# Performance work log

Measured on AMD Instinct MI355X. Metric: run time of the kernel, lower is better.

Reference implementation:

```python
import jax, jax.numpy as jnp
import numpy as np

B, Q, C = 128, 192, 512   # batch, num_queries (= num_targets per sample), num_classes
COST_CLASS = 1.0
BIG = jnp.float32(1e30)


def _lsap_col4row(cost):
    """Exact linear sum assignment (Jonker-Volgenant shortest augmenting path,
    same algorithm as scipy.optimize.linear_sum_assignment).
    cost: [n, n] float32. Returns col4row[i] = column assigned to row i (int32)."""
    n = cost.shape[0]

    def solve_row(cur_row, state):
        u, v, row4col, col4row = state

        # Dijkstra-like search for the shortest augmenting path from cur_row.
        def dj_cond(s):
            return s[6] < 0  # sink not found yet

        def dj_body(s):
            i, minVal, SR, SC, spc, path, sink = s
            SR = SR.at[i].set(True)
            r = minVal + cost[i] - u[i] - v          # reduced path costs, [n]
            upd = (~SC) & (r < spc)
            path = jnp.where(upd, i, path)
            spc = jnp.where(upd, r, spc)
            masked = jnp.where(SC, BIG, spc)
            j = jnp.argmin(masked).astype(jnp.int32)
            minVal = masked[j]
            SC = SC.at[j].set(True)
            unassigned = row4col[j] < 0
            sink = jnp.where(unassigned, j, jnp.int32(-1))
            i = jnp.where(unassigned, i, row4col[j])
            return i, minVal, SR, SC, spc, path, sink

        init = (jnp.asarray(cur_row, jnp.int32), jnp.float32(0.0),
                jnp.zeros(n, bool), jnp.zeros(n, bool),
                jnp.full(n, BIG, jnp.float32), jnp.zeros(n, jnp.int32),
                jnp.int32(-1))
        _, minVal, SR, SC, spc, path, sink = jax.lax.while_loop(dj_cond, dj_body, init)

        # Dual variable updates.
        u = u.at[cur_row].add(minVal)
        others = SR & (jnp.arange(n) != cur_row)   # assigned rows visited in the search
        u = u + jnp.where(others, minVal - spc[col4row], 0.0)
        v = v - jnp.where(SC, minVal - spc, 0.0)

        # Augment along the stored path from sink back to cur_row.
        def aug_cond(s):
            return ~s[3]

        def aug_body(s):
            j, r4c, c4r, _ = s
            i = path[j]
            r4c = r4c.at[j].set(i)
            nj = c4r[i]
            c4r = c4r.at[i].set(j)
            return nj, r4c, c4r, i == cur_row

        _, row4col, col4row, _ = jax.lax.while_loop(
            aug_cond, aug_body, (sink, row4col, col4row, jnp.bool_(False)))
        return u, v, row4col, col4row

    state = (jnp.zeros(n, jnp.float32), jnp.zeros(n, jnp.float32),
             jnp.full(n, -1, jnp.int32), jnp.full(n, -1, jnp.int32))
    _, _, _, col4row = jax.lax.fori_loop(0, n, solve_row, state)
    return col4row


def _match(predictions, targets):
    """BipartiteMatching: cost[b,q,j] = -softmax(pred)[b,q,targets[b,j]];
    per-sample Hungarian. Returns col4row: [B, Q] (row q matched to target col)."""
    prob = jax.nn.softmax(predictions, axis=-1)            # [B,Q,C]
    tgt = targets.astype(jnp.int32)
    cost = -jax.vmap(lambda p, t: p[:, t])(prob, tgt)      # [B,Q,Q]
    return jax.vmap(_lsap_col4row)(COST_CLASS * cost)      # [B,Q]


def setup_inputs() -> dict:
    key = jax.random.key(0)
    k1, k2 = jax.random.split(key)
    predictions = jax.random.normal(k1, (B, Q, C), dtype=jnp.float32)
    targets = jax.random.randint(k2, (B, Q), 0, C).astype(jnp.int64)
    return {"predictions": predictions, "targets": targets}


def reference(predictions, targets):
    # Matching is done under no_grad in the original module.
    col4row = _match(jax.lax.stop_gradient(predictions), targets)          # [B,Q]
    # Since matching is square, every query is matched; the num_classes fill
    # in the original is always fully overwritten.
    target_classes = jnp.take_along_axis(targets, col4row.astype(targets.dtype), axis=1)
    logp = jax.nn.log_softmax(predictions, axis=-1)                        # [B,Q,C]
    nll = -jnp.take_along_axis(logp, target_classes[..., None].astype(jnp.int32), axis=-1)
    return jnp.mean(nll)  # F.cross_entropy with default mean reduction over B*Q
```

## Files before the change

### kernel.cpp

```cpp
#include <hip/hip_runtime.h>
#include <math.h>


#define BB 128
#define QQ 192
#define CC 512
#define NBIG 1e30f

template<int CTRL>
__device__ __forceinline__ int dpp_mov(int x) {
    return __builtin_amdgcn_update_dpp(x, x, CTRL, 0xf, 0xf, false);
}

__device__ __forceinline__ int readlane_i(int v, int l) {
    return __builtin_amdgcn_readlane(v, l);
}
__device__ __forceinline__ float readlane_f(float v, int l) {
    return __int_as_float(__builtin_amdgcn_readlane(__float_as_int(v), l));
}
__device__ __forceinline__ unsigned umin_(unsigned a, unsigned b) { return a < b ? a : b; }

__device__ __forceinline__ float wave_max64(float x) {
    x = fmaxf(x, __int_as_float(dpp_mov<0x111>(__float_as_int(x))));
    x = fmaxf(x, __int_as_float(dpp_mov<0x112>(__float_as_int(x))));
    x = fmaxf(x, __int_as_float(dpp_mov<0x114>(__float_as_int(x))));
    x = fmaxf(x, __int_as_float(dpp_mov<0x118>(__float_as_int(x))));
    x = fmaxf(x, __int_as_float(dpp_mov<0x142>(__float_as_int(x))));
    x = fmaxf(x, __int_as_float(dpp_mov<0x143>(__float_as_int(x))));
    return __int_as_float(__builtin_amdgcn_readlane(__float_as_int(x), 63));
}
__device__ __forceinline__ float wave_sum64(float x) {
    x += __int_as_float(dpp_mov<0x111>(__float_as_int(x)));
    x += __int_as_float(dpp_mov<0x112>(__float_as_int(x)));
    x += __int_as_float(dpp_mov<0x114>(__float_as_int(x)));
    x += __int_as_float(dpp_mov<0x118>(__float_as_int(x)));
    x += __int_as_float(dpp_mov<0x142>(__float_as_int(x)));
    x += __int_as_float(dpp_mov<0x143>(__float_as_int(x)));
    return __int_as_float(__builtin_amdgcn_readlane(__float_as_int(x), 63));
}

__device__ __forceinline__ unsigned wave_min_pk(unsigned x) {
    x = umin_(x, (unsigned)dpp_mov<0x111>((int)x));
    x = umin_(x, (unsigned)dpp_mov<0x112>((int)x));
    x = umin_(x, (unsigned)dpp_mov<0x114>((int)x));
    x = umin_(x, (unsigned)dpp_mov<0x118>((int)x));
    unsigned a = (unsigned)readlane_i((int)x, 15);
    unsigned b = (unsigned)readlane_i((int)x, 31);
    unsigned c = (unsigned)readlane_i((int)x, 47);
    unsigned d = (unsigned)readlane_i((int)x, 63);
    return umin_(umin_(a, b), umin_(c, d));
}

__device__ __forceinline__ unsigned fkey(float f) {
    unsigned b = __float_as_uint(f);
    return b ^ (((unsigned)((int)b >> 31)) | 0x80000000u);
}

#define GET_I3(a, idx) readlane_i((((idx)>>6)==0) ? a##0 : ((((idx)>>6)==1) ? a##1 : a##2), (idx)&63)
#define GET_F3(a, idx) readlane_f((((idx)>>6)==0) ? a##0 : ((((idx)>>6)==1) ? a##1 : a##2), (idx)&63)
#define SET_I3(a, idx, val) do { const int _s=(idx)>>6, _l=(idx)&63; \
    if (_s==0) { if (lane==_l) a##0=(val); } \
    else if (_s==1) { if (lane==_l) a##1=(val); } \
    else { if (lane==_l) a##2=(val); } } while(0)

__launch_bounds__(256)
__global__ void hungarian_kernel(const float* __restrict__ pred,
                                 const int* __restrict__ targets,
                                 float* __restrict__ ws_part) {
    const int b = blockIdx.x;
    const int lane = threadIdx.x & 63;
    const int wv = threadIdx.x >> 6;

    extern __shared__ float smem[];
    float* cost    = smem;
    float* spc_lds = cost + QQ * QQ;
    float* lse_lds = spc_lds + QQ;
    int*   tgt_lds = (int*)(lse_lds + QQ);

    const int t0 = targets[b * QQ + lane];
    const int t1 = targets[b * QQ + lane + 64];
    const int t2 = targets[b * QQ + lane + 128];
    if (wv == 0) { tgt_lds[lane] = t0; tgt_lds[lane + 64] = t1; tgt_lds[lane + 128] = t2; }

    const float* predb = pred + (size_t)b * QQ * CC;
    {
        const int q0 = wv * 48, q1 = q0 + 48;
        float x[8];
        #pragma unroll
        for (int k = 0; k < 8; k++) x[k] = predb[(size_t)q0 * CC + lane + 64 * k];
        for (int q = q0; q < q1; q++) {
            const float* row = predb + (size_t)q * CC;
            float g0 = row[t0], g1 = row[t1], g2 = row[t2];
            float xn[8];
            if (q + 1 < q1) {
                const float* nrow = row + CC;
                #pragma unroll
                for (int k = 0; k < 8; k++) xn[k] = nrow[lane + 64 * k];
            }
            float mx = x[0];
            #pragma unroll
            for (int k = 1; k < 8; k++) mx = fmaxf(mx, x[k]);
            mx = wave_max64(mx);
            float s = 0.f;
            #pragma unroll
            for (int k = 0; k < 8; k++) s += expf(x[k] - mx);
            s = wave_sum64(s);
            float lse = mx + logf(s);
            if (lane == 0) lse_lds[q] = lse;
            cost[q * QQ + lane]       = -expf(g0 - lse);
            cost[q * QQ + lane + 64]  = -expf(g1 - lse);
            cost[q * QQ + lane + 128] = -expf(g2 - lse);
            #pragma unroll
            for (int k = 0; k < 8; k++) x[k] = xn[k];
        }
    }
    __syncthreads();
    if (wv != 0) return;

    float u0 = 0.f, u1 = 0.f, u2 = 0.f;
    float v0 = 0.f, v1 = 0.f, v2 = 0.f;
    int   c0 = -1, c1 = -1, c2 = -1;
    int   r0 = -1, r1 = -1, r2 = -1;

    for (int cur = 0; cur < QQ; cur++) {
        float spc0 = NBIG, spc1 = NBIG, spc2 = NBIG;
        int   p0 = 0, p1 = 0, p2 = 0;
        int   sc0 = 0, sc1 = 0, sc2 = 0;
        unsigned long long SRm0 = 0, SRm1 = 0, SRm2 = 0;
        int   i = cur;
        float minVal = 0.f;
        int   sink;

        while (true) {
            {
                const int is = i >> 6, il = i & 63;
                if (is == 0)      SRm0 |= 1ull << il;
                else if (is == 1) SRm1 |= 1ull << il;
                else              SRm2 |= 1ull << il;
            }
            const float* crow = cost + i * QQ;
            const float cA = crow[lane];
            const float cB = crow[lane + 64];
            const float cD = crow[lane + 128];
            const float ui = GET_F3(u, i);

            float rA = ((minVal + cA) - ui) - v0;  rA = sc0 ? NBIG : rA;
            if (rA < spc0) { spc0 = rA; p0 = i; }
            float rB = ((minVal + cB) - ui) - v1;  rB = sc1 ? NBIG : rB;
            if (rB < spc1) { spc1 = rB; p1 = i; }
            float rD = ((minVal + cD) - ui) - v2;  rD = sc2 ? NBIG : rD;
            if (rD < spc2) { spc2 = rD; p2 = i; }

            unsigned pkA = sc0 ? 0xFFFFFFFFu : ((fkey(spc0) & 0xFFFFFF00u) | (unsigned)lane);
            unsigned pkB = sc1 ? 0xFFFFFFFFu : ((fkey(spc1) & 0xFFFFFF00u) | (unsigned)(lane + 64));
            unsigned pkD = sc2 ? 0xFFFFFFFFu : ((fkey(spc2) & 0xFFFFFF00u) | (unsigned)(lane + 128));
            const unsigned pk = wave_min_pk(umin_(umin_(pkA, pkB), pkD));
            const int jstar = (int)(pk & 255u);
            const int os = jstar >> 6, ol = jstar & 63;

            minVal = readlane_f(os == 0 ? spc0 : (os == 1 ? spc1 : spc2), ol);
            sc0 |= (jstar == lane);
            sc1 |= (jstar == lane + 64);
            sc2 |= (jstar == lane + 128);
            const int rj = readlane_i(os == 0 ? r0 : (os == 1 ? r1 : r2), ol);
            if (rj < 0) { sink = jstar; break; }
            i = rj;
        }

        u0 += (cur == lane) ? minVal : 0.f;
        u1 += (cur == lane + 64) ? minVal : 0.f;
        u2 += (cur == lane + 128) ? minVal : 0.f;
        spc_lds[lane] = spc0; spc_lds[lane + 64] = spc1; spc_lds[lane + 128] = spc2;
        const int f0 = (int)((SRm0 >> lane) & 1ull);
        const int f1 = (int)((SRm1 >> lane) & 1ull);
        const int f2 = (int)((SRm2 >> lane) & 1ull);
        if (f0 && lane != cur)         u0 += minVal - spc_lds[c0];
        if (f1 && (lane + 64) != cur)  u1 += minVal - spc_lds[c1];
        if (f2 && (lane + 128) != cur) u2 += minVal - spc_lds[c2];
        if (sc0) v0 -= (minVal - spc0);
        if (sc1) v1 -= (minVal - spc1);
        if (sc2) v2 -= (minVal - spc2);

        int j = sink;
        while (true) {
            const int pj = GET_I3(p, j);
            SET_I3(r, j, pj);
            const int nj = GET_I3(c, pj);
            SET_I3(c, pj, j);
            if (pj == cur) break;
            j = nj;
        }
    }

    float part = 0.f;
    {
        const int tc0 = tgt_lds[c0], tc1 = tgt_lds[c1], tc2 = tgt_lds[c2];
        part += lse_lds[lane]       - predb[(size_t)lane * CC + tc0];
        part += lse_lds[lane + 64]  - predb[(size_t)(lane + 64) * CC + tc1];
        part += lse_lds[lane + 128] - predb[(size_t)(lane + 128) * CC + tc2];
    }
    part = wave_sum64(part);
    if (lane == 0) ws_part[b] = part;
}

__launch_bounds__(64)
__global__ void reduce_kernel(const float* __restrict__ ws_part,
                              float* __restrict__ out) {
    int lane = threadIdx.x;
    float s = ws_part[lane] + ws_part[lane + 64];
    s = wave_sum64(s);
    if (lane == 0) out[0] = s / (float)(BB * QQ);
}

extern "C" void kernel_launch(void* const* d_in, const int* in_sizes, int n_in,
                              void* d_out, int out_size, void* d_ws, size_t ws_size,
                              hipStream_t stream) {
    const float* pred = (const float*)d_in[0];
    const int* targets = (const int*)d_in[1];
    float* out = (float*)d_out;
    float* ws = (float*)d_ws;

    const int lds_bytes = (QQ * QQ + 3 * QQ) * (int)sizeof(float);

    hipLaunchKernelGGL(hungarian_kernel, dim3(BB), dim3(256), lds_bytes, stream,
                       pred, targets, ws);
    hipLaunchKernelGGL(reduce_kernel, dim3(1), dim3(64), 0, stream, ws, out);
}
```

Baseline: 837.1 us.

## Pack assigned-row index into argmin key to remove readlanes on critical path

The Dijkstra inner loop now keeps a per-column packed key that carries the column's assigned row plus one in its low byte. A single wave min-reduction therefore yields the next row directly, without dependent readlanes of the row4col registers. The minVal readlane and the SC marking are deferred into the next iteration using ballots on matching keys. The reduced-cost arithmetic is also refactored to hoist the shared minVal-ui term. This shortens the serial dependency chain per step, at the cost of extra ballots and changed tie-breaking (the low bits now hold row ids instead of column ids), which could alter the assignment when keys tie.

```diff
diff --git a/kernel.cpp b/kernel.cpp
--- a/kernel.cpp
+++ b/kernel.cpp
@@ -119,17 +119,22 @@
 
     float u0 = 0.f, u1 = 0.f, u2 = 0.f;
     float v0 = 0.f, v1 = 0.f, v2 = 0.f;
-    int   c0 = -1, c1 = -1, c2 = -1;
-    int   r0 = -1, r1 = -1, r2 = -1;
+    int   xx0 = -1, xx1 = -1, xx2 = -1;
+    int   yy0 = -1, yy1 = -1, yy2 = -1;
 
     for (int cur = 0; cur < QQ; cur++) {
         float spc0 = NBIG, spc1 = NBIG, spc2 = NBIG;
         int   p0 = 0, p1 = 0, p2 = 0;
         int   sc0 = 0, sc1 = 0, sc2 = 0;
+        unsigned k0 = 0xFFFFFFFFu, k1 = 0xFFFFFFFFu, k2 = 0xFFFFFFFFu;
         unsigned long long SRm0 = 0, SRm1 = 0, SRm2 = 0;
+        const unsigned yf0 = (unsigned)(yy0 + 1);
+        const unsigned yf1 = (unsigned)(yy1 + 1);
+        const unsigned yf2 = (unsigned)(yy2 + 1);
         int   i = cur;
         float minVal = 0.f;
         int   sink;
+        unsigned mn = 0xFFFFFFFFu;
 
         while (true) {
             {
@@ -142,29 +147,49 @@
             const float cA = crow[lane];
             const float cB = crow[lane + 64];
             const float cD = crow[lane + 128];
+
+            if (mn != 0xFFFFFFFFu) {
+                const int m0 = (k0 == mn), m1 = (k1 == mn), m2 = (k2 == mn);
+                const unsigned long long b0 = __ballot(m0);
+                const unsigned long long b1 = __ballot(m1);
+                const unsigned long long b2 = __ballot(m2);
+                if (b0)      minVal = readlane_f(spc0, __ffsll(b0) - 1);
+                else if (b1) minVal = readlane_f(spc1, __ffsll(b1) - 1);
+                else         minVal = readlane_f(spc2, __ffsll(b2) - 1);
+                sc0 |= m0; sc1 |= m1; sc2 |= m2;
+                k0 = m0 ? 0xFFFFFFFFu : k0;
+                k1 = m1 ? 0xFFFFFFFFu : k1;
+                k2 = m2 ? 0xFFFFFFFFu : k2;
+            }
             const float ui = GET_F3(u, i);
-
-            float rA = ((minVal + cA) - ui) - v0;  rA = sc0 ? NBIG : rA;
+            const float fs = minVal - ui;
+            const float sv0 = sc0 ? NBIG : fs - v0;
+            const float sv1 = sc1 ? NBIG : fs - v1;
+            const float sv2 = sc2 ? NBIG : fs - v2;
+
+            const float rA = cA + sv0;
+            const float rB = cB + sv1;
+            const float rD = cD + sv2;
             if (rA < spc0) { spc0 = rA; p0 = i; }
-            float rB = ((minVal + cB) - ui) - v1;  rB = sc1 ? NBIG : rB;
             if (rB < spc1) { spc1 = rB; p1 = i; }
-            float rD = ((minVal + cD) - ui) - v2;  rD = sc2 ? NBIG : rD;
             if (rD < spc2) { spc2 = rD; p2 = i; }
-
-            unsigned pkA = sc0 ? 0xFFFFFFFFu : ((fkey(spc0) & 0xFFFFFF00u) | (unsigned)lane);
-            unsigned pkB = sc1 ? 0xFFFFFFFFu : ((fkey(spc1) & 0xFFFFFF00u) | (unsigned)(lane + 64));
-            unsigned pkD = sc2 ? 0xFFFFFFFFu : ((fkey(spc2) & 0xFFFFFF00u) | (unsigned)(lane + 128));
-            const unsigned pk = wave_min_pk(umin_(umin_(pkA, pkB), pkD));
-            const int jstar = (int)(pk & 255u);
-            const int os = jstar >> 6, ol = jstar & 63;
-
-            minVal = readlane_f(os == 0 ? spc0 : (os == 1 ? spc1 : spc2), ol);
-            sc0 |= (jstar == lane);
-            sc1 |= (jstar == lane + 64);
-            sc2 |= (jstar == lane + 128);
-            const int rj = readlane_i(os == 0 ? r0 : (os == 1 ? r1 : r2), ol);
-            if (rj < 0) { sink = jstar; break; }
-            i = rj;
+            k0 = umin_(k0, (fkey(rA) & 0xFFFFFF00u) | yf0);
+            k1 = umin_(k1, (fkey(rB) & 0xFFFFFF00u) | yf1);
+            k2 = umin_(k2, (fkey(rD) & 0xFFFFFF00u) | yf2);
+
+            mn = wave_min_pk(umin_(umin_(k0, k1), k2));
+            const int rjf = (int)(mn & 255u);
+            if (rjf == 0) {
+                const unsigned long long b0 = __ballot(k0 == mn);
+                const unsigned long long b1 = __ballot(k1 == mn);
+                const unsigned long long b2 = __ballot(k2 == mn);
+                int ol;
+                if (b0)      { ol = __ffsll(b0) - 1; sink = ol;       minVal = readlane_f(spc0, ol); }
+                else if (b1) { ol = __ffsll(b1) - 1; sink = ol + 64;  minVal = readlane_f(spc1, ol); }
+                else         { ol = __ffsll(b2) - 1; sink = ol + 128; minVal = readlane_f(spc2, ol); }
+                break;
+            }
+            i = rjf - 1;
         }
 
         u0 += (cur == lane) ? minVal : 0.f;
@@ -174,9 +199,9 @@
         const int f0 = (int)((SRm0 >> lane) & 1ull);
         const int f1 = (int)((SRm1 >> lane) & 1ull);
         const int f2 = (int)((SRm2 >> lane) & 1ull);
-        if (f0 && lane != cur)         u0 += minVal - spc_lds[c0];
-        if (f1 && (lane + 64) != cur)  u1 += minVal - spc_lds[c1];
-        if (f2 && (lane + 128) != cur) u2 += minVal - spc_lds[c2];
+        if (f0 && lane != cur)         u0 += minVal - spc_lds[xx0];
+        if (f1 && (lane + 64) != cur)  u1 += minVal - spc_lds[xx1];
+        if (f2 && (lane + 128) != cur) u2 += minVal - spc_lds[xx2];
         if (sc0) v0 -= (minVal - spc0);
         if (sc1) v1 -= (minVal - spc1);
         if (sc2) v2 -= (minVal - spc2);
@@ -184,9 +209,9 @@
         int j = sink;
         while (true) {
             const int pj = GET_I3(p, j);
-            SET_I3(r, j, pj);
-            const int nj = GET_I3(c, pj);
-            SET_I3(c, pj, j);
+            SET_I3(yy, j, pj);
+            const int nj = GET_I3(xx, pj);
+            SET_I3(xx, pj, j);
             if (pj == cur) break;
             j = nj;
         }
@@ -194,7 +219,7 @@
 
     float part = 0.f;
     {
-        const int tc0 = tgt_lds[c0], tc1 = tgt_lds[c1], tc2 = tgt_lds[c2];
+        const int tc0 = tgt_lds[xx0], tc1 = tgt_lds[xx1], tc2 = tgt_lds[xx2];
         part += lse_lds[lane]       - predb[(size_t)lane * CC + tc0];
         part += lse_lds[lane + 64]  - predb[(size_t)(lane + 64) * CC + tc1];
         part += lse_lds[lane + 128] - predb[(size_t)(lane + 128) * CC + tc2];
```

New measurement: 904.0 us. 1.08x slower.
